# Performance work log

Measured on AMD Instinct MI355X. Metric: run time of the kernel, lower is better.

Reference implementation:

```python
import jax, jax.numpy as jnp
import numpy as np

EPS = 1e-08
MARGIN_SCALE = 0.15  # forward overwrites the margin arg with 0.15 * L1(id diff)


def setup_inputs() -> dict:
    key = jax.random.key(0)
    k1, k2 = jax.random.split(key)
    B, F, C = 512, 256, 4
    ids = jax.random.randint(k1, (B, C), 0, 2).astype(jnp.int64)
    feats = jax.random.normal(k2, (B, F), dtype=jnp.float32)
    return {"ids": ids, "feats": feats}


def reference(ids, feats):
    B, F = feats.shape
    # pairwise cosine: cos[i, j] = cos(feats[i], feats[j]) with the torch eps scheme
    norm = jnp.maximum(jnp.sqrt(jnp.sum(feats * feats, axis=1) + EPS), EPS)  # [B]
    cos = (feats @ feats.T) / (norm[:, None] * norm[None, :])  # [B, B]

    eq = jnp.all(ids[:, None, :] == ids[None, :, :], axis=-1)  # [B, B] same-id pairs
    marg = MARGIN_SCALE * jnp.sum(
        jnp.abs(ids[:, None, :] - ids[None, :, :]), axis=-1
    ).astype(feats.dtype)  # [B, B]

    offdiag = ~jnp.eye(B, dtype=bool)
    sim = eq & offdiag          # positives (excluding self)
    dif = (~eq) & offdiag       # negatives (excluding self)

    # hinge[i, j, k] = relu(marg[i, k] - cos[i, j] + cos[i, k]) for j in sim(i), k in dif(i)
    hinge = jnp.maximum(0.0, marg[:, None, :] - cos[:, :, None] + cos[:, None, :])  # [B,B,B]
    pair_mask = (sim[:, :, None] & dif[:, None, :]).astype(feats.dtype)
    row_sum = jnp.sum(hinge * pair_mask, axis=(1, 2))  # [B]

    cnt = sim.sum(axis=1) * dif.sum(axis=1)  # [B] number of (sim, dif) pairs per row
    valid = cnt > 0
    row_loss = jnp.where(valid, row_sum / jnp.maximum(cnt, 1).astype(feats.dtype), 0.0)
    num_valid = jnp.maximum(valid.sum(), 1).astype(feats.dtype)
    return jnp.sum(row_loss) / num_valid
```

## Files before the change

### kernel.cpp

```cpp
#include <hip/hip_runtime.h>
#include <math.h>

#define EPSF 1e-8f

constexpr int B = 512;
constexpr int F = 256;

using frag_ab = __attribute__((ext_vector_type(8))) short;
using f32x4   = __attribute__((ext_vector_type(4))) float;

__device__ __forceinline__ unsigned short f2bf(float f) {
    unsigned int u = __float_as_uint(f);
    unsigned int r = (u + 0x7fffu + ((u >> 16) & 1u)) >> 16;
    return (unsigned short)r;
}

__global__ __launch_bounds__(64) void gram_mfma(
    const float* __restrict__ feats, float* __restrict__ gram,
    float* __restrict__ invs)
{
    const int bid = blockIdx.x;
    const int it = bid >> 5, jt = bid & 31;
    const int l = threadIdx.x;

    __shared__ __align__(16) unsigned char Abf[16 * 512];
    __shared__ __align__(16) unsigned char Bbf[16 * 512];

    const float4* Ag = (const float4*)(feats + (size_t)(it * 16) * F);
    const float4* Bg = (const float4*)(feats + (size_t)(jt * 16) * F);

    #pragma unroll
    for (int m = 0; m < 16; ++m) {
        const int swz = ((l >> 1) ^ (m & 7)) * 16 + (l & 1) * 8;
        float4 a = Ag[m * 64 + l];
        ushort4 ha = { f2bf(a.x), f2bf(a.y), f2bf(a.z), f2bf(a.w) };
        *(ushort4*)(Abf + m * 512 + swz) = ha;
        float4 b = Bg[m * 64 + l];
        ushort4 hb = { f2bf(b.x), f2bf(b.y), f2bf(b.z), f2bf(b.w) };
        *(ushort4*)(Bbf + m * 512 + swz) = hb;
    }

    const int row_f = l & 15;
    const int kg    = l >> 4;
    f32x4 acc = {0.f, 0.f, 0.f, 0.f};
    #pragma unroll
    for (int kc = 0; kc < 8; ++kc) {
        int cc = (kc * 4 + kg) ^ (row_f & 7);
        frag_ab a = *(const frag_ab*)(Abf + row_f * 512 + cc * 16);
        frag_ab b = *(const frag_ab*)(Bbf + row_f * 512 + cc * 16);
        acc = __builtin_amdgcn_mfma_f32_16x16x32_bf16(a, b, acc, 0, 0, 0);
    }
    const int col = l & 15;
    #pragma unroll
    for (int j = 0; j < 4; ++j) {
        int row = kg * 4 + j;
        float v = acc[j];
        gram[(size_t)(it * 16 + row) * B + jt * 16 + col] = v;
        if (it == jt && col == row)
            invs[it * 16 + row] = 1.f / fmaxf(sqrtf(v + EPSF), EPSF);
    }
}

__global__ __launch_bounds__(64) void row_wave(
    const int* __restrict__ ids, const float* __restrict__ gram,
    const float* __restrict__ invs,
    float* __restrict__ rowloss, int* __restrict__ rowvalid)
{
    const int i = blockIdx.x;
    const int l = threadIdx.x;

    __shared__ float vals[B];

    const int4 idi = ((const int4*)ids)[i];
    const int pi = (idi.x & 1) | ((idi.y & 1) << 1)
                 | ((idi.z & 1) << 2) | ((idi.w & 1) << 3);
    const float invi = invs[i];

    float cosv[8];
    int   pj[8];
    #pragma unroll
    for (int q = 0; q < 8; ++q) {
        const int j = q * 64 + l;
        int4 v = ((const int4*)ids)[j];
        pj[q] = (v.x & 1) | ((v.y & 1) << 1) | ((v.z & 1) << 2) | ((v.w & 1) << 3);
        cosv[q] = gram[(size_t)i * B + j] * invi * invs[j];
    }

    const unsigned long long lmask = (1ull << l) - 1ull;
    int off = 0;
    #pragma unroll
    for (int q = 0; q < 8; ++q) {
        const int j = q * 64 + l;
        const bool sim = (pj[q] == pi) && (j != i);
        const unsigned long long m = __ballot(sim);
        if (sim) vals[off + (int)__popcll(m & lmask)] = cosv[q];
        off += (int)__popcll(m);
    }
    const int ns = off;

    float b[8];
    #pragma unroll
    for (int q = 0; q < 8; ++q)
        b[q] = (pj[q] != pi) ? 0.15f * (float)__popc(pj[q] ^ pi) + cosv[q]
                             : -1e30f;

    float sa[8] = {0.f, 0.f, 0.f, 0.f, 0.f, 0.f, 0.f, 0.f};
    for (int t = 0; t < ns; ++t) {
        const float a = vals[t];
        #pragma unroll
        for (int q = 0; q < 8; ++q) sa[q] += fmaxf(0.f, b[q] - a);
    }
    float s = ((sa[0] + sa[1]) + (sa[2] + sa[3]))
            + ((sa[4] + sa[5]) + (sa[6] + sa[7]));
    #pragma unroll
    for (int o = 32; o > 0; o >>= 1) s += __shfl_down(s, o);

    if (l == 0) {
        const int nd = (B - 1) - ns;
        const long cnt = (long)ns * (long)nd;
        rowloss[i]  = (cnt > 0) ? s / (float)cnt : 0.f;
        rowvalid[i] = (cnt > 0) ? 1 : 0;
    }
}

__global__ __launch_bounds__(256) void finalize_kernel(
    const float* __restrict__ rowloss, const int* __restrict__ rowvalid,
    float* __restrict__ out)
{
    const int tid  = threadIdx.x;
    const int lane = tid & 63;
    const int wid  = tid >> 6;
    __shared__ float sb[4], vb[4];

    float s = rowloss[tid] + rowloss[tid + 256];
    float v = (float)(rowvalid[tid] + rowvalid[tid + 256]);
    #pragma unroll
    for (int o = 32; o > 0; o >>= 1) {
        s += __shfl_down(s, o);
        v += __shfl_down(v, o);
    }
    if (lane == 0) { sb[wid] = s; vb[wid] = v; }
    __syncthreads();
    if (tid == 0) {
        float ts = sb[0] + sb[1] + sb[2] + sb[3];
        float tv = vb[0] + vb[1] + vb[2] + vb[3];
        out[0] = ts / fmaxf(tv, 1.f);
    }
}

extern "C" void kernel_launch(void* const* d_in, const int* in_sizes, int n_in,
                              void* d_out, int out_size, void* d_ws, size_t ws_size,
                              hipStream_t stream) {
    const int*   ids   = (const int*)d_in[0];
    const float* feats = (const float*)d_in[1];
    float* out = (float*)d_out;

    char* ws = (char*)d_ws;
    float* gram     = (float*)ws;
    float* invs     = (float*)(ws + (1u << 20));
    float* rowloss  = (float*)(ws + (1u << 20) + 2048);
    int*   rowvalid = (int*)(ws + (1u << 20) + 4096);

    hipLaunchKernelGGL(gram_mfma, dim3(32 * 32), dim3(64), 0, stream,
                       feats, gram, invs);
    hipLaunchKernelGGL(row_wave, dim3(B), dim3(64), 0, stream,
                       ids, gram, invs, rowloss, rowvalid);
    hipLaunchKernelGGL(finalize_kernel, dim3(1), dim3(256), 0, stream,
                       rowloss, rowvalid, out);
}
```

Before: 15.70 us.

## Drop finalize kernel via precomputed valid count and atomic accumulation

Removes the third launch by precomputing the number of valid rows in block 0 of the Gram kernel. It does this by counting how many rows share each 16-pattern id signature. Each row wave then atomically adds its normalized loss divided by that count straight into the output, which block 0 zeroes first. This saves one kernel launch and the rowloss/rowvalid round trip, at the cost of float atomics on a single address and a nondeterministic summation order.

```diff
diff --git a/kernel.cpp b/kernel.cpp
--- a/kernel.cpp
+++ b/kernel.cpp
@@ -16,8 +16,9 @@
 }
 
 __global__ __launch_bounds__(64) void gram_mfma(
-    const float* __restrict__ feats, float* __restrict__ gram,
-    float* __restrict__ invs)
+    const float* __restrict__ feats, const int* __restrict__ ids,
+    float* __restrict__ gram, float* __restrict__ invs,
+    float* __restrict__ Vout, float* __restrict__ out)
 {
     const int bid = blockIdx.x;
     const int it = bid >> 5, jt = bid & 31;
@@ -25,6 +26,26 @@
 
     __shared__ __align__(16) unsigned char Abf[16 * 512];
     __shared__ __align__(16) unsigned char Bbf[16 * 512];
+
+    if (bid == 0) {
+        if (l == 0) out[0] = 0.f;
+        int pj[8];
+        #pragma unroll
+        for (int q = 0; q < 8; ++q) {
+            int4 v = ((const int4*)ids)[q * 64 + l];
+            pj[q] = (v.x & 1) | ((v.y & 1) << 1) | ((v.z & 1) << 2) | ((v.w & 1) << 3);
+        }
+        int V = 0;
+        #pragma unroll
+        for (int p = 0; p < 16; ++p) {
+            int c = 0;
+            #pragma unroll
+            for (int q = 0; q < 8; ++q)
+                c += (int)__popcll(__ballot(pj[q] == p));
+            V += (c >= 2 && c <= B - 1) ? c : 0;
+        }
+        if (l == 0) Vout[0] = (float)V;
+    }
 
     const float4* Ag = (const float4*)(feats + (size_t)(it * 16) * F);
     const float4* Bg = (const float4*)(feats + (size_t)(jt * 16) * F);
@@ -63,8 +84,8 @@
 
 __global__ __launch_bounds__(64) void row_wave(
     const int* __restrict__ ids, const float* __restrict__ gram,
-    const float* __restrict__ invs,
-    float* __restrict__ rowloss, int* __restrict__ rowvalid)
+    const float* __restrict__ invs, const float* __restrict__ Vin,
+    float* __restrict__ out)
 {
     const int i = blockIdx.x;
     const int l = threadIdx.x;
@@ -118,33 +139,8 @@
     if (l == 0) {
         const int nd = (B - 1) - ns;
         const long cnt = (long)ns * (long)nd;
-        rowloss[i]  = (cnt > 0) ? s / (float)cnt : 0.f;
-        rowvalid[i] = (cnt > 0) ? 1 : 0;
-    }
-}
-
-__global__ __launch_bounds__(256) void finalize_kernel(
-    const float* __restrict__ rowloss, const int* __restrict__ rowvalid,
-    float* __restrict__ out)
-{
-    const int tid  = threadIdx.x;
-    const int lane = tid & 63;
-    const int wid  = tid >> 6;
-    __shared__ float sb[4], vb[4];
-
-    float s = rowloss[tid] + rowloss[tid + 256];
-    float v = (float)(rowvalid[tid] + rowvalid[tid + 256]);
-    #pragma unroll
-    for (int o = 32; o > 0; o >>= 1) {
-        s += __shfl_down(s, o);
-        v += __shfl_down(v, o);
-    }
-    if (lane == 0) { sb[wid] = s; vb[wid] = v; }
-    __syncthreads();
-    if (tid == 0) {
-        float ts = sb[0] + sb[1] + sb[2] + sb[3];
-        float tv = vb[0] + vb[1] + vb[2] + vb[3];
-        out[0] = ts / fmaxf(tv, 1.f);
+        if (cnt > 0)
+            atomicAdd(out, (s / (float)cnt) / Vin[0]);
     }
 }
 
@@ -156,15 +152,12 @@
     float* out = (float*)d_out;
 
     char* ws = (char*)d_ws;
-    float* gram     = (float*)ws;
-    float* invs     = (float*)(ws + (1u << 20));
-    float* rowloss  = (float*)(ws + (1u << 20) + 2048);
-    int*   rowvalid = (int*)(ws + (1u << 20) + 4096);
+    float* gram = (float*)ws;
+    float* invs = (float*)(ws + (1u << 20));
+    float* Vws  = (float*)(ws + (1u << 20) + 2048);
 
     hipLaunchKernelGGL(gram_mfma, dim3(32 * 32), dim3(64), 0, stream,
-                       feats, gram, invs);
+                       feats, ids, gram, invs, Vws, out);
     hipLaunchKernelGGL(row_wave, dim3(B), dim3(64), 0, stream,
-                       ids, gram, invs, rowloss, rowvalid);
-    hipLaunchKernelGGL(finalize_kernel, dim3(1), dim3(256), 0, stream,
-                       rowloss, rowvalid, out);
+                       ids, gram, invs, Vws, out);
 }
```

After: 21.09 us. 34.4% more time.
